# Optimization experiments

Hardware: AMD Instinct MI355X
Metric: run time of the kernel (lower is better)

Reference implementation:

```python
import jax, jax.numpy as jnp
import numpy as np

FORGET_BIAS = 1.0  # TF LSTMCell default


def _lstm_scan(z_tm, c0, m0, W, b, P):
    """Projected LSTM over time-major z_tm (T, B, I). Returns (T, B, num_proj)."""
    def step(carry, x):
        c, m = carry
        gates = jnp.concatenate([x, m], axis=-1) @ W + b  # (B, 4*S)
        i, j, f, o = jnp.split(gates, 4, axis=-1)         # TF gate order i,j,f,o
        c = jax.nn.sigmoid(f + FORGET_BIAS) * c + jax.nn.sigmoid(i) * jnp.tanh(j)
        m = (jax.nn.sigmoid(o) * jnp.tanh(c)) @ P          # projected output/state
        return (c, m), m
    _, ms = jax.lax.scan(step, (c0, m0), z_tm)
    return ms


def setup_inputs() -> dict:
    key = jax.random.key(0)
    ks = jax.random.split(key, 10)
    B, T, I, S, F = 128, 400, 100, 100, 200
    sc_w = 1.0 / np.sqrt(I + F)
    sc_p = 1.0 / np.sqrt(S)
    return {
        "z": jax.random.normal(ks[0], (B, T, I), dtype=jnp.float32),
        "c_f0": jax.random.normal(ks[1], (B, S), dtype=jnp.float32),
        "m_f0": jax.random.normal(ks[2], (B, F), dtype=jnp.float32),
        "c_b0": jax.random.normal(ks[3], (B, S), dtype=jnp.float32),
        "m_b0": jax.random.normal(ks[4], (B, F), dtype=jnp.float32),
        "W_f": jax.random.normal(ks[5], (I + F, 4 * S), dtype=jnp.float32) * sc_w,
        "b_f": jnp.zeros((4 * S,), dtype=jnp.float32),
        "P_f": jax.random.normal(ks[6], (S, F), dtype=jnp.float32) * sc_p,
        "W_b": jax.random.normal(ks[7], (I + F, 4 * S), dtype=jnp.float32) * sc_w,
        "b_b": jnp.zeros((4 * S,), dtype=jnp.float32),
        "P_b": jax.random.normal(ks[8], (S, F), dtype=jnp.float32) * sc_p,
    }


def reference(z, c_f0, m_f0, c_b0, m_b0, W_f, b_f, P_f, W_b, b_b, P_b):
    B = z.shape[0]
    z_tm = jnp.transpose(z, (1, 0, 2))                      # (T, B, I)
    out_f = _lstm_scan(z_tm, c_f0, m_f0, W_f, b_f, P_f)     # (T, B, F)
    out_b = _lstm_scan(z_tm[::-1], c_b0, m_b0, W_b, b_b, P_b)[::-1]
    out = jnp.concatenate([out_f, out_b], axis=-1)          # (T, B, 2F)
    # TF: concat of per-step (B, 2F) outputs along axis=1 -> (B, T*2F)
    return jnp.transpose(out, (1, 0, 2)).reshape(B, -1)
```

## Files before the change

kernel.cpp:

```cpp
#include <hip/hip_runtime.h>
#include <stdint.h>

#define TB     400
#define OUTROW 160000

typedef _Float16 half2_t __attribute__((ext_vector_type(2)));
typedef _Float16 f16x8 __attribute__((ext_vector_type(8)));
typedef float    f32x4 __attribute__((ext_vector_type(4)));
typedef uint16_t u16;
typedef uint32_t u32;

__device__ __forceinline__ float sigf(float x){ return 1.0f/(1.0f+__expf(-x)); }
__device__ __forceinline__ float tanhf_(float x){ float e=__expf(2.0f*x); return 1.0f-2.0f/(e+1.0f); }
__device__ __forceinline__ u16 h16(float x){ _Float16 h=(_Float16)x; return __builtin_bit_cast(u16,h); }
__device__ __forceinline__ u32 pk2(float a, float b){ return (u32)h16(a) | ((u32)h16(b)<<16); }
__device__ __forceinline__ float f16f(u16 u){ return (float)__builtin_bit_cast(_Float16,u); }
__device__ __forceinline__ float dot2f(u32 w, u32 x, float acc){
  return __builtin_amdgcn_fdot2(__builtin_bit_cast(half2_t,w), __builtin_bit_cast(half2_t,x), acc, false);
}
__device__ __forceinline__ float qxor1(float x){
  return __builtin_bit_cast(float, __builtin_amdgcn_mov_dpp(__builtin_bit_cast(int,x), 0xB1, 0xf, 0xf, true));
}
__device__ __forceinline__ float qxor2(float x){
  return __builtin_bit_cast(float, __builtin_amdgcn_mov_dpp(__builtin_bit_cast(int,x), 0x4E, 0xf, 0xf, true));
}

__global__ __launch_bounds__(512)
void k_prep(const float* __restrict__ Wf, const float* __restrict__ Pf,
            const float* __restrict__ Wb, const float* __restrict__ Pb,
            const float* __restrict__ m0f, const float* __restrict__ m0b,
            u32* __restrict__ Qp, float* __restrict__ M0W)
{
  const int b = blockIdx.x, tid = threadIdx.x;
  if (b < 104){
    const int dir = b/52, j = b%52;
    const float* W = dir?Wb:Wf; const float* P = dir?Pb:Pf;
    __shared__ float pr[2][200];
    for (int i=tid;i<400;i+=512){ int u=i/200,k=i%200; int hk=2*j+u;
      pr[u][k] = (hk<100)? P[(size_t)hk*200+k] : 0.f; }
    __syncthreads();
    if (tid<400){
      float a0=0.f,a1=0.f;
      for (int k=0;k<200;++k){ float w = W[(size_t)(100+k)*400+tid]; a0 += pr[0][k]*w; a1 += pr[1][k]*w; }
      Qp[(size_t)(dir*52+j)*400+tid] = pk2(a0,a1);
    }
  } else {
    const int bb2 = b-104, dir = bb2>>7, seq = bb2&127;
    const float* m0 = dir?m0b:m0f; const float* W = dir?Wb:Wf;
    __shared__ float mr[200];
    if (tid<200) mr[tid] = m0[(size_t)seq*200+tid];
    __syncthreads();
    if (tid<400){
      float a=0.f;
      for (int k=0;k<200;++k) a += mr[k]*W[(size_t)(100+k)*400+tid];
      M0W[(size_t)bb2*400+tid] = a;
    }
  }
}

__global__ __launch_bounds__(512, 1)
void k_g4(const float* __restrict__ z,
          const float* __restrict__ Wf, const float* __restrict__ bf,
          const float* __restrict__ Wb, const float* __restrict__ bb,
          const float* __restrict__ M0W, u16* __restrict__ Gh)
{
  __shared__ __align__(16) u16 xa[5][4][512];
  const int tid = threadIdx.x, wv = tid>>6, lane = tid&63;
  const int l15 = lane&15, lg = lane>>4;
  const int dir = blockIdx.x>>7, seq = blockIdx.x&127;
  const float* W  = dir?Wb:Wf;
  const float* bv = dir?bb:bf;

  const int nnt = (wv==0)?4:3;
  const int ntl[4] = {wv, wv+8, wv+16, 24};

  f16x8 wb_[4][4];
  float bias[4], m0w[4];
  #pragma unroll
  for (int i=0;i<4;++i) if (i<nnt){
    const int col = ntl[i]*16 + l15;
    #pragma unroll
    for (int kt=0;kt<4;++kt){
      f16x8 v;
      #pragma unroll
      for (int e=0;e<8;++e){
        int k = kt*32 + lg*8 + e;
        v[e] = (_Float16)((k<100)? W[(size_t)k*400+col] : 0.f);
      }
      wb_[i][kt]=v;
    }
    bias[i] = bv[col] + (((col/100)==2)?1.0f:0.0f);
    m0w[i]  = M0W[(size_t)(dir*128+seq)*400 + col];
  }
  const int tfirst = dir?(TB-1):0;

  for (int i=tid;i<10240;i+=512) ((u16*)xa)[i] = (u16)0;
  __syncthreads();

  for (int chunk=0; chunk<5; ++chunk){
    for (int i=tid;i<8000;i+=512){
      int r = i/100, k = i%100;
      int t = chunk*80 + r;
      float v = z[(size_t)seq*40000 + (size_t)t*100 + k];
      int mt = r>>4, m = r&15, kt = k>>5, kk = k&31;
      xa[mt][kt][(m|((kk>>3)<<4))*8 + (kk&7)] = h16(v);
    }
    __syncthreads();
    #pragma unroll
    for (int mt=0; mt<5; ++mt){
      f16x8 af[4];
      #pragma unroll
      for (int kt=0;kt<4;++kt)
        af[kt] = *reinterpret_cast<const f16x8*>(&xa[mt][kt][lane*8]);
      #pragma unroll
      for (int i=0;i<4;++i) if (i<nnt){
        f32x4 acc = {0.f,0.f,0.f,0.f};
        #pragma unroll
        for (int kt=0;kt<4;++kt)
          acc = __builtin_amdgcn_mfma_f32_16x16x32_f16(af[kt], wb_[i][kt], acc, 0,0,0);
        const int col = ntl[i]*16 + l15;
        #pragma unroll
        for (int r=0;r<4;++r){
          int t = chunk*80 + mt*16 + lg*4 + r;
          float gv = acc[r] + bias[i] + ((t==tfirst)? m0w[i] : 0.f);
          Gh[((size_t)dir*51200 + (size_t)seq*400 + t)*400 + col] = h16(gv);
        }
      }
    }
    __syncthreads();
  }
}

__global__ __launch_bounds__(704, 1)
void k_rec6(const float* __restrict__ c0f, const float* __restrict__ c0b,
            const float* __restrict__ Pf, const float* __restrict__ Pb,
            const u32* __restrict__ Qp, const u16* __restrict__ Gh,
            float* __restrict__ out)
{
  __shared__ __align__(16) u32 h2[2][52];
  const int tid = threadIdx.x, dir = blockIdx.x>>7, seq = blockIdx.x&127;
  const float* c0 = dir?c0b:c0f;
  const float* P  = dir?Pb:Pf;
  const int s = tid>>2, g = tid&3;
  const int c = g*100 + s;

  uint4 wq[13];
  float cs = 0.f;
  if (tid < 400){
    #pragma unroll
    for (int q=0;q<13;++q){
      wq[q].x = Qp[(size_t)(dir*52+4*q+0)*400 + c];
      wq[q].y = Qp[(size_t)(dir*52+4*q+1)*400 + c];
      wq[q].z = Qp[(size_t)(dir*52+4*q+2)*400 + c];
      wq[q].w = Qp[(size_t)(dir*52+4*q+3)*400 + c];
    }
    cs = c0[(size_t)seq*100 + s];
  }
  const int pc = tid - 448;
  uint4 pw[13];
  if (pc >= 0 && pc < 200){
    #pragma unroll
    for (int q=0;q<13;++q){
      u32 r[4];
      #pragma unroll
      for (int u=0;u<4;++u){
        int j = 4*q+u;
        r[u] = (j<50)? pk2(P[(size_t)(2*j)*200+pc], P[(size_t)(2*j+1)*200+pc]) : 0u;
      }
      pw[q] = make_uint4(r[0],r[1],r[2],r[3]);
    }
  }
  if (tid < 104) ((u32*)h2)[tid] = 0u;
  __syncthreads();

  const u16* gptr = Gh + ((size_t)dir*51200 + (size_t)seq*400 + (dir?(TB-1):0))*400 + c;
  const intptr_t gstep = dir ? -400 : 400;
  u16 gn = 0;
  if (tid<400) gn = *gptr;

  for (int t=0; t<=TB; ++t){
    const int p = t&1;
    if (tid < 400 && t < TB){
      u16 gc = gn;
      gptr += gstep;
      if (t+1 < TB) gn = *gptr;
      float a0=0.f,a1=0.f,a2=0.f,a3=0.f;
      #pragma unroll
      for (int q=0;q<13;++q){
        uint4 hv = *(const uint4*)(&h2[p][4*q]);
        a0=dot2f(wq[q].x,hv.x,a0); a1=dot2f(wq[q].y,hv.y,a1);
        a2=dot2f(wq[q].z,hv.z,a2); a3=dot2f(wq[q].w,hv.w,a3);
      }
      float a = ((a0+a1)+(a2+a3)) + f16f(gc);
      float arg = (g==1) ? a+a : a;
      float v = sigf(arg);
      float act = (g==1) ? 2.0f*v-1.0f : v;
      float bx = qxor1(act);
      float dx = qxor2(act);
      float ex = qxor2(bx);
      float I = (g==0)?act:(g==1)?bx:(g==2)?dx:ex;
      float J = (g==1)?act:(g==0)?bx:(g==3)?dx:ex;
      float F = (g==2)?act:(g==3)?bx:(g==0)?dx:ex;
      float O = (g==3)?act:(g==2)?bx:(g==1)?dx:ex;
      float cc = F*cs + I*J; cs = cc;
      float h = O*tanhf_(cc);
      if (g==0) ((u16*)&h2[p^1][0])[s] = h16(h);
    } else if (pc >= 0 && pc < 200 && t >= 1){
      float m0=0.f,m1=0.f,m2=0.f,m3=0.f;
      #pragma unroll
      for (int q=0;q<13;++q){
        uint4 hv = *(const uint4*)(&h2[p][4*q]);
        m0=dot2f(pw[q].x,hv.x,m0); m1=dot2f(pw[q].y,hv.y,m1);
        m2=dot2f(pw[q].z,hv.z,m2); m3=dot2f(pw[q].w,hv.w,m3);
      }
      const int tt = dir ? (TB-t) : (t-1);
      __builtin_nontemporal_store((m0+m1)+(m2+m3),
          out + (size_t)seq*OUTROW + (size_t)tt*400 + dir*200 + pc);
    }
    __syncthreads();
  }
}

extern "C" void kernel_launch(void* const* d_in, const int* in_sizes, int n_in,
                              void* d_out, int out_size, void* d_ws, size_t ws_size,
                              hipStream_t stream) {
  (void)in_sizes; (void)n_in; (void)out_size; (void)ws_size;
  const float* z   = (const float*)d_in[0];
  const float* c0f = (const float*)d_in[1];
  const float* m0f = (const float*)d_in[2];
  const float* c0b = (const float*)d_in[3];
  const float* m0b = (const float*)d_in[4];
  const float* Wf  = (const float*)d_in[5];
  const float* bf  = (const float*)d_in[6];
  const float* Pf  = (const float*)d_in[7];
  const float* Wb  = (const float*)d_in[8];
  const float* bb  = (const float*)d_in[9];
  const float* Pb  = (const float*)d_in[10];

  u32*   Qp  = (u32*)d_ws;
  float* M0W = (float*)((char*)d_ws + 196608);
  u16*   Gh  = (u16*)((char*)d_ws + 655360);

  k_prep<<<360, 512, 0, stream>>>(Wf, Pf, Wb, Pb, m0f, m0b, Qp, M0W);
  k_g4  <<<256, 512, 0, stream>>>(z, Wf, bf, Wb, bb, M0W, Gh);
  k_rec6<<<256, 704, 0, stream>>>(c0f, c0b, Pf, Pb, Qp, Gh, (float*)d_out);
}
```

Before: 323.5 us.

## Transpose gate buffer to column-major time and batch recurrent loads/stores by eight

The precomputed input-gate buffer is stored time-contiguous per gate column, so the GEMM kernel writes four packed halves per store. The recurrent kernel then fetches eight timesteps of gate input with one 16-byte load instead of one scalar load per step. The projection threads buffer eight outputs in registers and flush them together. In exchange the loop is unrolled by eight, which raises register pressure, and the final projection step is peeled out of the loop.

```diff
diff --git a/kernel.cpp b/kernel.cpp
--- a/kernel.cpp
+++ b/kernel.cpp
@@ -59,10 +59,10 @@
 }
 
 __global__ __launch_bounds__(512, 1)
-void k_g4(const float* __restrict__ z,
+void k_g5(const float* __restrict__ z,
           const float* __restrict__ Wf, const float* __restrict__ bf,
           const float* __restrict__ Wb, const float* __restrict__ bb,
-          const float* __restrict__ M0W, u16* __restrict__ Gh)
+          const float* __restrict__ M0W, u16* __restrict__ GhT)
 {
   __shared__ __align__(16) u16 xa[5][4][512];
   const int tid = threadIdx.x, wv = tid>>6, lane = tid&63;
@@ -119,12 +119,18 @@
         for (int kt=0;kt<4;++kt)
           acc = __builtin_amdgcn_mfma_f32_16x16x32_f16(af[kt], wb_[i][kt], acc, 0,0,0);
         const int col = ntl[i]*16 + l15;
+        const int t0 = chunk*80 + mt*16 + lg*4;
+        u16 pkv[4];
         #pragma unroll
         for (int r=0;r<4;++r){
-          int t = chunk*80 + mt*16 + lg*4 + r;
-          float gv = acc[r] + bias[i] + ((t==tfirst)? m0w[i] : 0.f);
-          Gh[((size_t)dir*51200 + (size_t)seq*400 + t)*400 + col] = h16(gv);
-        }
+          int t = t0 + r;
+          float gvf = acc[r] + bias[i] + ((t==tfirst)? m0w[i] : 0.f);
+          pkv[r] = h16(gvf);
+        }
+        uint2 wv2;
+        wv2.x = (u32)pkv[0] | ((u32)pkv[1]<<16);
+        wv2.y = (u32)pkv[2] | ((u32)pkv[3]<<16);
+        *(uint2*)(GhT + ((size_t)(dir*128+seq)*400 + col)*400 + t0) = wv2;
       }
     }
     __syncthreads();
@@ -132,13 +138,14 @@
 }
 
 __global__ __launch_bounds__(704, 1)
-void k_rec6(const float* __restrict__ c0f, const float* __restrict__ c0b,
+void k_rec8(const float* __restrict__ c0f, const float* __restrict__ c0b,
             const float* __restrict__ Pf, const float* __restrict__ Pb,
-            const u32* __restrict__ Qp, const u16* __restrict__ Gh,
+            const u32* __restrict__ Qp, const u16* __restrict__ GhT,
             float* __restrict__ out)
 {
   __shared__ __align__(16) u32 h2[2][52];
-  const int tid = threadIdx.x, dir = blockIdx.x>>7, seq = blockIdx.x&127;
+  const int tid = threadIdx.x;
+  const int dir = blockIdx.x>>7, seq = blockIdx.x&127;
   const float* c0 = dir?c0b:c0f;
   const float* P  = dir?Pb:Pf;
   const int s = tid>>2, g = tid&3;
@@ -173,51 +180,80 @@
   if (tid < 104) ((u32*)h2)[tid] = 0u;
   __syncthreads();
 
-  const u16* gptr = Gh + ((size_t)dir*51200 + (size_t)seq*400 + (dir?(TB-1):0))*400 + c;
-  const intptr_t gstep = dir ? -400 : 400;
-  u16 gn = 0;
-  if (tid<400) gn = *gptr;
-
-  for (int t=0; t<=TB; ++t){
-    const int p = t&1;
-    if (tid < 400 && t < TB){
-      u16 gc = gn;
-      gptr += gstep;
-      if (t+1 < TB) gn = *gptr;
-      float a0=0.f,a1=0.f,a2=0.f,a3=0.f;
-      #pragma unroll
-      for (int q=0;q<13;++q){
-        uint4 hv = *(const uint4*)(&h2[p][4*q]);
-        a0=dot2f(wq[q].x,hv.x,a0); a1=dot2f(wq[q].y,hv.y,a1);
-        a2=dot2f(wq[q].z,hv.z,a2); a3=dot2f(wq[q].w,hv.w,a3);
-      }
-      float a = ((a0+a1)+(a2+a3)) + f16f(gc);
-      float arg = (g==1) ? a+a : a;
-      float v = sigf(arg);
-      float act = (g==1) ? 2.0f*v-1.0f : v;
-      float bx = qxor1(act);
-      float dx = qxor2(act);
-      float ex = qxor2(bx);
-      float I = (g==0)?act:(g==1)?bx:(g==2)?dx:ex;
-      float J = (g==1)?act:(g==0)?bx:(g==3)?dx:ex;
-      float F = (g==2)?act:(g==3)?bx:(g==0)?dx:ex;
-      float O = (g==3)?act:(g==2)?bx:(g==1)?dx:ex;
-      float cc = F*cs + I*J; cs = cc;
-      float h = O*tanhf_(cc);
-      if (g==0) ((u16*)&h2[p^1][0])[s] = h16(h);
-    } else if (pc >= 0 && pc < 200 && t >= 1){
-      float m0=0.f,m1=0.f,m2=0.f,m3=0.f;
-      #pragma unroll
-      for (int q=0;q<13;++q){
-        uint4 hv = *(const uint4*)(&h2[p][4*q]);
-        m0=dot2f(pw[q].x,hv.x,m0); m1=dot2f(pw[q].y,hv.y,m1);
-        m2=dot2f(pw[q].z,hv.z,m2); m3=dot2f(pw[q].w,hv.w,m3);
-      }
-      const int tt = dir ? (TB-t) : (t-1);
-      __builtin_nontemporal_store((m0+m1)+(m2+m3),
+  const u16* gbase = GhT + ((size_t)(dir*128+seq)*400 + c)*400;
+  uint4 gv = make_uint4(0,0,0,0);
+  float mbuf[8];
+
+  for (int grp=0; grp<50; ++grp){
+    #pragma unroll
+    for (int u=0; u<8; ++u){
+      const int t = grp*8 + u;
+      const int p = t&1;
+      if (tid < 400){
+        if (u == 0){
+          const int t0 = dir ? (392 - t) : t;
+          gv = *(const uint4*)(gbase + t0);
+        }
+        const u16 gc = ((const u16*)&gv)[dir ? (7-u) : u];
+        float a0=0.f,a1=0.f,a2=0.f,a3=0.f;
+        #pragma unroll
+        for (int q=0;q<13;++q){
+          uint4 hv = *(const uint4*)(&h2[p][4*q]);
+          a0=dot2f(wq[q].x,hv.x,a0); a1=dot2f(wq[q].y,hv.y,a1);
+          a2=dot2f(wq[q].z,hv.z,a2); a3=dot2f(wq[q].w,hv.w,a3);
+        }
+        float a = ((a0+a1)+(a2+a3)) + f16f(gc);
+        float arg = (g==1) ? a+a : a;
+        float v = sigf(arg);
+        float act = (g==1) ? 2.0f*v-1.0f : v;
+        float bx = qxor1(act);
+        float dx = qxor2(act);
+        float ex = qxor2(bx);
+        float I = (g==0)?act:(g==1)?bx:(g==2)?dx:ex;
+        float J = (g==1)?act:(g==0)?bx:(g==3)?dx:ex;
+        float F = (g==2)?act:(g==3)?bx:(g==0)?dx:ex;
+        float O = (g==3)?act:(g==2)?bx:(g==1)?dx:ex;
+        float cc = F*cs + I*J; cs = cc;
+        float h = O*tanhf_(cc);
+        if (g==0) ((u16*)&h2[p^1][0])[s] = h16(h);
+      } else if (pc >= 0 && pc < 200 && t >= 1){
+        float m0=0.f,m1=0.f,m2=0.f,m3=0.f;
+        #pragma unroll
+        for (int q=0;q<13;++q){
+          uint4 hv = *(const uint4*)(&h2[p][4*q]);
+          m0=dot2f(pw[q].x,hv.x,m0); m1=dot2f(pw[q].y,hv.y,m1);
+          m2=dot2f(pw[q].z,hv.z,m2); m3=dot2f(pw[q].w,hv.w,m3);
+        }
+        const int mi = t-1;
+        mbuf[mi&7] = (m0+m1)+(m2+m3);
+        if ((mi&7) == 7){
+          const int mb = mi & ~7;
+          #pragma unroll
+          for (int e=0;e<8;++e){
+            const int tt = dir ? (TB-1-(mb+e)) : (mb+e);
+            __builtin_nontemporal_store(mbuf[e],
+                out + (size_t)seq*OUTROW + (size_t)tt*400 + dir*200 + pc);
+          }
+        }
+      }
+      __syncthreads();
+    }
+  }
+  if (pc >= 0 && pc < 200){
+    float m0=0.f,m1=0.f,m2=0.f,m3=0.f;
+    #pragma unroll
+    for (int q=0;q<13;++q){
+      uint4 hv = *(const uint4*)(&h2[0][4*q]);
+      m0=dot2f(pw[q].x,hv.x,m0); m1=dot2f(pw[q].y,hv.y,m1);
+      m2=dot2f(pw[q].z,hv.z,m2); m3=dot2f(pw[q].w,hv.w,m3);
+    }
+    mbuf[7] = (m0+m1)+(m2+m3);
+    #pragma unroll
+    for (int e=0;e<8;++e){
+      const int tt = dir ? (TB-1-(392+e)) : (392+e);
+      __builtin_nontemporal_store(mbuf[e],
           out + (size_t)seq*OUTROW + (size_t)tt*400 + dir*200 + pc);
     }
-    __syncthreads();
   }
 }
 
@@ -239,9 +275,9 @@
 
   u32*   Qp  = (u32*)d_ws;
   float* M0W = (float*)((char*)d_ws + 196608);
-  u16*   Gh  = (u16*)((char*)d_ws + 655360);
+  u16*   GhT = (u16*)((char*)d_ws + 655360);
 
   k_prep<<<360, 512, 0, stream>>>(Wf, Pf, Wb, Pb, m0f, m0b, Qp, M0W);
-  k_g4  <<<256, 512, 0, stream>>>(z, Wf, bf, Wb, bb, M0W, Gh);
-  k_rec6<<<256, 704, 0, stream>>>(c0f, c0b, Pf, Pb, Qp, Gh, (float*)d_out);
-}
+  k_g5  <<<256, 512, 0, stream>>>(z, Wf, bf, Wb, bb, M0W, GhT);
+  k_rec8<<<256, 704, 0, stream>>>(c0f, c0b, Pf, Pb, Qp, GhT, (float*)d_out);
+}
```

Result: slower. 336.8 us (+4.1%).
